# Performance work log

Hardware: AMD Instinct MI355X
Metric: run time of the kernel (lower is better)

Reference implementation:

```python
import jax, jax.numpy as jnp
import numpy as np

N_U, N_O = 20000, 10000      # rows in users / orders
C = 256                      # channels
TXT = 1536                   # text_embed_dim
NNUM, NCAT, NTXT = 3, 3, 1   # columns per stype (same for both tables)
NCOLS = NNUM + NCAT + NTXT   # 7 columns per table
VOCAB = 101                  # num_cats + 1
E = 10000                    # edges (orders -> users fkey)
MAXP = 16                    # max_parents


def setup_inputs() -> dict:
    key = jax.random.key(0)
    ks = jax.random.split(key, 24)
    s = 0.02
    return {
        "users_num": jax.random.normal(ks[0], (N_U, NNUM), jnp.float32),
        "users_cat": jax.random.randint(ks[1], (N_U, NCAT), 0, VOCAB),
        "users_text": jax.random.normal(ks[2], (N_U, NTXT, TXT), jnp.float32),
        "orders_num": jax.random.normal(ks[3], (N_O, NNUM), jnp.float32),
        "orders_cat": jax.random.randint(ks[4], (N_O, NCAT), 0, VOCAB),
        "orders_text": jax.random.normal(ks[5], (N_O, NTXT, TXT), jnp.float32),
        "edge_index": jax.random.randint(ks[6], (2, E), 0, N_O),
        "table_emb": jax.random.normal(ks[7], (2, C), jnp.float32) * s,
        # users params
        "u_num_w": jax.random.normal(ks[8], (NNUM, C), jnp.float32) * s,
        "u_num_b": jax.random.normal(ks[9], (NNUM, C), jnp.float32) * s,
        "u_cat_tab": jax.random.normal(ks[10], (NCAT, VOCAB, C), jnp.float32) * s,
        "u_txt_w": jax.random.normal(ks[11], (NTXT, C, TXT), jnp.float32) * s,
        "u_txt_b": jax.random.normal(ks[12], (NTXT, C), jnp.float32) * s,
        "u_col": jax.random.normal(ks[13], (NCOLS, C), jnp.float32) * s,
        # orders params
        "o_num_w": jax.random.normal(ks[14], (NNUM, C), jnp.float32) * s,
        "o_num_b": jax.random.normal(ks[15], (NNUM, C), jnp.float32) * s,
        "o_cat_tab": jax.random.normal(ks[16], (NCAT, VOCAB, C), jnp.float32) * s,
        "o_txt_w": jax.random.normal(ks[17], (NTXT, C, TXT), jnp.float32) * s,
        "o_txt_b": jax.random.normal(ks[18], (NTXT, C), jnp.float32) * s,
        "o_col": jax.random.normal(ks[19], (NCOLS, C), jnp.float32) * s,
    }


def _table_tokens(num, cat, txt, nw, nb, ctab, tw, tb, col, temb):
    # num: [N, NNUM]; nw/nb: [NNUM, C] -> per-col Linear(1, C) + SiLU
    tn = jax.nn.silu(num[:, :, None] * nw[None] + nb[None])        # [N, NNUM, C]
    # per-col Embedding lookup: ctab [NCAT, V, C], cat [N, NCAT]
    tc = ctab[jnp.arange(ctab.shape[0])[None, :], cat]             # [N, NCAT, C]
    # per-col Linear(TXT, C): tw [NTXT, C, TXT]
    tt = jnp.einsum('nkt,kct->nkc', txt, tw) + tb[None]            # [N, NTXT, C]
    tok = jnp.concatenate([tn, tc, tt], axis=1) + col[None] + temb  # [N, NCOLS, C]
    # original concatenates per-column blocks of N rows each -> (cols, N, C) flatten
    return tok.transpose(1, 0, 2).reshape(-1, tok.shape[-1])


def reference(users_num, users_cat, users_text, orders_num, orders_cat, orders_text,
              edge_index, table_emb,
              u_num_w, u_num_b, u_cat_tab, u_txt_w, u_txt_b, u_col,
              o_num_w, o_num_b, o_cat_tab, o_txt_w, o_txt_b, o_col):
    xu = _table_tokens(users_num, users_cat, users_text,
                       u_num_w, u_num_b, u_cat_tab, u_txt_w, u_txt_b, u_col, table_emb[0])
    xo = _table_tokens(orders_num, orders_cat, orders_text,
                       o_num_w, o_num_b, o_cat_tab, o_txt_w, o_txt_b, o_col, table_emb[1])
    x = jnp.concatenate([xu, xo], axis=0)                           # [S, C]

    node_idxs = jnp.concatenate([jnp.tile(jnp.arange(N_U), NCOLS),
                                 jnp.tile(jnp.arange(N_U, N_U + N_O), NCOLS)])
    col_idxs = jnp.concatenate([jnp.repeat(jnp.arange(NCOLS), N_U),
                                jnp.repeat(jnp.arange(NCOLS, 2 * NCOLS), N_O)])
    table_idxs = jnp.concatenate([jnp.zeros(NCOLS * N_U, jnp.int32),
                                  jnp.ones(NCOLS * N_O, jnp.int32)])

    # f2p neighbor build: first MAXP parents per child node, in edge order
    num_nodes = N_U + N_O
    child = edge_index[0] + N_U    # orders offset = N_U
    parent = edge_index[1]         # users offset = 0
    order = jnp.argsort(child, stable=True)
    cs, ps = child[order], parent[order]
    seg_start = jnp.searchsorted(cs, cs, side='left')
    rank = jnp.arange(E) - seg_start                                # position within child's group
    valid = rank < MAXP
    tbl = jnp.full((num_nodes + 1, MAXP), -1, dtype=ps.dtype)
    tbl = tbl.at[jnp.where(valid, cs, num_nodes), jnp.minimum(rank, MAXP - 1)].set(
        jnp.where(valid, ps, -1))
    f2p_nbr_idxs = tbl[:num_nodes][node_idxs]                       # [S, MAXP]

    return (x, node_idxs, col_idxs, table_idxs, f2p_nbr_idxs, num_nodes)
```

## Files before the change

kernel.cpp:

```cpp
#include <hip/hip_runtime.h>
#include <hip/hip_bf16.h>

typedef __bf16 bf16;
typedef __bf16 bf16x8 __attribute__((ext_vector_type(8)));
typedef float f32x4 __attribute__((ext_vector_type(4)));

#define NU 20000
#define NO 10000
#define CDIM 256
#define TDIM 1536
#define EN 10000
#define VOCAB 101
#define MAXP 16
#define CAP 32

#define NODE_OFF 53760000LL
#define COL_OFF  53970000LL
#define TAB_OFF  54180000LL
#define F2P_OFF  54390000LL
#define NN_OFF   57750000LL

#define GEMM_U_BLKS 314
#define GEMM_O_BLKS 158
#define MISC_BLKS   22500
#define IDX_BLKS    840
#define MISC_OFF    (GEMM_U_BLKS + GEMM_O_BLKS)
#define IDX_OFF     (MISC_OFF + MISC_BLKS)
#define TOTAL_BLKS  (IDX_OFF + IDX_BLKS)

__global__ void edges_fill(const int* __restrict__ edge, int* __restrict__ counts,
                           unsigned long long* __restrict__ pairs)
{
    int e = blockIdx.x * 256 + threadIdx.x;
    if (e >= EN) return;
    int child = edge[e];
    unsigned parent = (unsigned)edge[EN + e];
    int slot = atomicAdd(&counts[child], 1);
    if (slot < CAP)
        pairs[child * CAP + slot] = ((unsigned long long)(unsigned)e << 32) | parent;
}

__global__ void build_tbl(const int* __restrict__ counts,
                          const unsigned long long* __restrict__ pairs,
                          int* __restrict__ tbl)
{
    int mm = blockIdx.x * 256 + threadIdx.x;
    if (mm >= NO) return;
    int cnt = counts[mm];
    if (cnt > CAP) cnt = CAP;
    unsigned long long v[CAP];
    for (int i = 0; i < cnt; i++) v[i] = pairs[mm * CAP + i];
    for (int i = 1; i < cnt; i++) {
        unsigned long long key = v[i];
        int j = i - 1;
        while (j >= 0 && v[j] > key) { v[j + 1] = v[j]; j--; }
        v[j + 1] = key;
    }
#pragma unroll
    for (int j = 0; j < MAXP; j++)
        tbl[mm * MAXP + j] = (j < cnt) ? (int)(v[j] & 0xffffffffULL) : -1;
}

__device__ __forceinline__ void idx_body(int iblk, const int* __restrict__ tbl,
                                         float* __restrict__ out)
{
    int i = iblk * 256 + threadIdx.x;
    if (i >= 210000) return;
    float nodev, colvf, tabv;
    int m = -1;
    if (i < 140000) {
        int n = i % 20000;
        nodev = (float)n; colvf = (float)(i / 20000); tabv = 0.f;
    } else {
        int i2 = i - 140000;
        m = i2 % 10000;
        nodev = (float)(20000 + m); colvf = (float)(7 + i2 / 10000); tabv = 1.f;
    }
    out[NODE_OFF + i] = nodev;
    out[COL_OFF + i]  = colvf;
    out[TAB_OFF + i]  = tabv;

    float h[16];
    if (m < 0) {
#pragma unroll
        for (int j = 0; j < 16; j++) h[j] = -1.f;
    } else {
#pragma unroll
        for (int j = 0; j < 16; j++) h[j] = (float)tbl[m * MAXP + j];
    }
    float4* dst = (float4*)&out[F2P_OFF + (long long)i * 16];
#pragma unroll
    for (int j = 0; j < 4; j++)
        dst[j] = *(const float4*)&h[j * 4];
    if (i == 0) out[NN_OFF] = 30000.f;
}

__device__ __forceinline__ void misc_body(int mb,
    const float* __restrict__ unum, const int* __restrict__ ucat,
    const float* __restrict__ onum, const int* __restrict__ ocat,
    const float* __restrict__ temb,
    const float* __restrict__ unw, const float* __restrict__ unb,
    const float* __restrict__ uctab, const float* __restrict__ ucol,
    const float* __restrict__ onw, const float* __restrict__ onb,
    const float* __restrict__ octab, const float* __restrict__ ocol,
    float* __restrict__ out)
{
    int t = threadIdx.x;
    int ridx = mb * 8 + (t >> 5);
    int c0 = (t & 31) * 8;
    bool isU = ridx < 120000;
    int k, n; long long orow;
    const float *num, *nw, *nb, *ctab, *colw, *te;
    const int* cat;
    if (isU) {
        k = ridx / 20000; n = ridx - k * 20000; orow = ridx;
        num = unum; cat = ucat; nw = unw; nb = unb; ctab = uctab; colw = ucol; te = temb;
    } else {
        int i2 = ridx - 120000;
        k = i2 / 10000; n = i2 - k * 10000; orow = (long long)ridx + 20000;
        num = onum; cat = ocat; nw = onw; nb = onb; ctab = octab; colw = ocol; te = temb + CDIM;
    }
    float colv[8], tev[8];
    *(float4*)&colv[0] = *(const float4*)&colw[k * CDIM + c0];
    *(float4*)&colv[4] = *(const float4*)&colw[k * CDIM + c0 + 4];
    *(float4*)&tev[0]  = *(const float4*)&te[c0];
    *(float4*)&tev[4]  = *(const float4*)&te[c0 + 4];
    float res[8];
    if (k < 3) {
        float v = num[n * 3 + k];
        float wv[8], bv[8];
        *(float4*)&wv[0] = *(const float4*)&nw[k * CDIM + c0];
        *(float4*)&wv[4] = *(const float4*)&nw[k * CDIM + c0 + 4];
        *(float4*)&bv[0] = *(const float4*)&nb[k * CDIM + c0];
        *(float4*)&bv[4] = *(const float4*)&nb[k * CDIM + c0 + 4];
#pragma unroll
        for (int j = 0; j < 8; j++) {
            float x = v * wv[j] + bv[j];
            float s = x / (1.f + __expf(-x));
            res[j] = s + colv[j] + tev[j];
        }
    } else {
        int cv = cat[n * 3 + (k - 3)];
        float tcv[8];
        *(float4*)&tcv[0] = *(const float4*)&ctab[((k - 3) * VOCAB + cv) * CDIM + c0];
        *(float4*)&tcv[4] = *(const float4*)&ctab[((k - 3) * VOCAB + cv) * CDIM + c0 + 4];
#pragma unroll
        for (int j = 0; j < 8; j++)
            res[j] = tcv[j] + colv[j] + tev[j];
    }
    *(float4*)&out[orow * CDIM + c0]     = *(const float4*)&res[0];
    *(float4*)&out[orow * CDIM + c0 + 4] = *(const float4*)&res[4];
}

__device__ __forceinline__ void gemm_body(
    const float* __restrict__ A, const float* __restrict__ W,
    const float* __restrict__ tbias, const float* __restrict__ colw,
    const float* __restrict__ temb, float* __restrict__ out,
    int M, long long out_row_base, int mblk, int nblk,
    bf16* As, bf16* Bs)
{
    constexpr int BK = 64, LDA = 72;
    const int tid = threadIdx.x;
    const int m0 = mblk * 128;
    const int n0 = nblk * 128;
    const int w = tid >> 6, lane = tid & 63;
    const int wm = (w & 1) * 64, wn = (w >> 1) * 64;
    const int lrow = lane & 15, lquad = lane >> 4;

    f32x4 acc[4][4];
#pragma unroll
    for (int a = 0; a < 4; a++)
#pragma unroll
        for (int b = 0; b < 4; b++) acc[a][b] = (f32x4){0.f, 0.f, 0.f, 0.f};

    for (int k0 = 0; k0 < TDIM; k0 += BK) {
        __syncthreads();
#pragma unroll
        for (int i = 0; i < 8; i++) {
            int c = tid + i * 256;
            int row = c >> 4;
            int col4 = (c & 15) << 2;
            int ga = m0 + row; if (ga >= M) ga = M - 1;
            float4 av = *(const float4*)&A[(size_t)ga * TDIM + k0 + col4];
            __attribute__((aligned(8))) bf16 ha[4] =
                {(bf16)av.x, (bf16)av.y, (bf16)av.z, (bf16)av.w};
            *(unsigned long long*)&As[row * LDA + col4] = *(const unsigned long long*)ha;
            float4 bv = *(const float4*)&W[(size_t)(n0 + row) * TDIM + k0 + col4];
            __attribute__((aligned(8))) bf16 hb[4] =
                {(bf16)bv.x, (bf16)bv.y, (bf16)bv.z, (bf16)bv.w};
            *(unsigned long long*)&Bs[row * LDA + col4] = *(const unsigned long long*)hb;
        }
        __syncthreads();
#pragma unroll
        for (int ks = 0; ks < 2; ks++) {
            bf16x8 afr[4], bfr[4];
#pragma unroll
            for (int mi = 0; mi < 4; mi++)
                afr[mi] = *(const bf16x8*)&As[(wm + mi * 16 + lrow) * LDA + ks * 32 + lquad * 8];
#pragma unroll
            for (int ni = 0; ni < 4; ni++)
                bfr[ni] = *(const bf16x8*)&Bs[(wn + ni * 16 + lrow) * LDA + ks * 32 + lquad * 8];
#pragma unroll
            for (int mi = 0; mi < 4; mi++)
#pragma unroll
                for (int ni = 0; ni < 4; ni++)
                    acc[mi][ni] = __builtin_amdgcn_mfma_f32_16x16x32_bf16(
                        afr[mi], bfr[ni], acc[mi][ni], 0, 0, 0);
        }
    }

#pragma unroll
    for (int ni = 0; ni < 4; ni++) {
        int c = n0 + wn + ni * 16 + lrow;
        float bias = tbias[c] + colw[6 * CDIM + c] + temb[c];
#pragma unroll
        for (int mi = 0; mi < 4; mi++) {
            int mbase = m0 + wm + mi * 16 + lquad * 4;
#pragma unroll
            for (int r = 0; r < 4; r++) {
                int m = mbase + r;
                if (m < M)
                    out[(out_row_base + m) * CDIM + c] = acc[mi][ni][r] + bias;
            }
        }
    }
}

__global__ __launch_bounds__(256) void mega(
    const float* __restrict__ users_num, const int* __restrict__ users_cat,
    const float* __restrict__ users_text,
    const float* __restrict__ orders_num, const int* __restrict__ orders_cat,
    const float* __restrict__ orders_text,
    const float* __restrict__ temb,
    const float* __restrict__ unw, const float* __restrict__ unb,
    const float* __restrict__ uctab, const float* __restrict__ utw,
    const float* __restrict__ utb, const float* __restrict__ ucol,
    const float* __restrict__ onw, const float* __restrict__ onb,
    const float* __restrict__ octab, const float* __restrict__ otw,
    const float* __restrict__ otb, const float* __restrict__ ocol,
    const int* __restrict__ tbl, float* __restrict__ out)
{
    __shared__ bf16 As[128 * 72];
    __shared__ bf16 Bs[128 * 72];
    int b = blockIdx.x;
    if (b < GEMM_U_BLKS) {
        gemm_body(users_text, utw, utb, ucol, temb, out,
                  NU, 120000LL, b >> 1, b & 1, As, Bs);
    } else if (b < MISC_OFF) {
        int bb = b - GEMM_U_BLKS;
        gemm_body(orders_text, otw, otb, ocol, temb + CDIM, out,
                  NO, 200000LL, bb >> 1, bb & 1, As, Bs);
    } else if (b < IDX_OFF) {
        misc_body(b - MISC_OFF, users_num, users_cat, orders_num, orders_cat,
                  temb, unw, unb, uctab, ucol, onw, onb, octab, ocol, out);
    } else {
        idx_body(b - IDX_OFF, tbl, out);
    }
}

extern "C" void kernel_launch(void* const* d_in, const int* in_sizes, int n_in,
                              void* d_out, int out_size, void* d_ws, size_t ws_size,
                              hipStream_t stream)
{
    const float* users_num   = (const float*)d_in[0];
    const int*   users_cat   = (const int*)d_in[1];
    const float* users_text  = (const float*)d_in[2];
    const float* orders_num  = (const float*)d_in[3];
    const int*   orders_cat  = (const int*)d_in[4];
    const float* orders_text = (const float*)d_in[5];
    const int*   edge_index  = (const int*)d_in[6];
    const float* table_emb   = (const float*)d_in[7];
    const float* u_num_w   = (const float*)d_in[8];
    const float* u_num_b   = (const float*)d_in[9];
    const float* u_cat_tab = (const float*)d_in[10];
    const float* u_txt_w   = (const float*)d_in[11];
    const float* u_txt_b   = (const float*)d_in[12];
    const float* u_col     = (const float*)d_in[13];
    const float* o_num_w   = (const float*)d_in[14];
    const float* o_num_b   = (const float*)d_in[15];
    const float* o_cat_tab = (const float*)d_in[16];
    const float* o_txt_w   = (const float*)d_in[17];
    const float* o_txt_b   = (const float*)d_in[18];
    const float* o_col     = (const float*)d_in[19];
    float* out = (float*)d_out;

    int* counts = (int*)d_ws;
    unsigned long long* pairs = (unsigned long long*)((char*)d_ws + 65536);
    int* tbl = (int*)((char*)d_ws + 65536 + (size_t)NO * CAP * 8);

    hipMemsetAsync(counts, 0, NO * sizeof(int), stream);
    edges_fill<<<(EN + 255) / 256, 256, 0, stream>>>(edge_index, counts, pairs);
    build_tbl<<<(NO + 255) / 256, 256, 0, stream>>>(counts, pairs, tbl);
    mega<<<TOTAL_BLKS, 256, 0, stream>>>(
        users_num, users_cat, users_text, orders_num, orders_cat, orders_text,
        table_emb, u_num_w, u_num_b, u_cat_tab, u_txt_w, u_txt_b, u_col,
        o_num_w, o_num_b, o_cat_tab, o_txt_w, o_txt_b, o_col, tbl, out);
}
```

Before: 479.6 us.

## Pre-convert text and weights to bf16 and stream GEMM tiles via direct LDS loads

A new prep kernel converts the user and order text activations and the text weights from fp32 to bf16 in workspace, fused with the edge-fill step. The GEMM then loads bf16 tiles straight into LDS with global_load_lds, so it no longer converts in registers during the main loop and reads half the bytes. The cost is an extra pass that reads the full fp32 text once and writes a bf16 copy of roughly 90 MB. The old fp32 path is kept as a fallback for when the workspace is too small.

```diff
diff --git a/kernel.cpp b/kernel.cpp
--- a/kernel.cpp
+++ b/kernel.cpp
@@ -28,10 +28,26 @@
 #define IDX_OFF     (MISC_OFF + MISC_BLKS)
 #define TOTAL_BLKS  (IDX_OFF + IDX_BLKS)
 
-__global__ void edges_fill(const int* __restrict__ edge, int* __restrict__ counts,
-                           unsigned long long* __restrict__ pairs)
-{
-    int e = blockIdx.x * 256 + threadIdx.x;
+#define P_EDGE  40
+#define P_CVU   (P_EDGE + 7500)
+#define P_CVO   (P_CVU + 3750)
+#define P_CVWU  (P_CVO + 96)
+#define P_CVWO  (P_CVWU + 96)
+#define PREP_BLKS P_CVWO
+
+#define WS_PAIRS_OFF 65536ULL
+#define WS_TBL_OFF   (WS_PAIRS_OFF + (unsigned long long)NO * CAP * 8)
+#define WS_AB_U_OFF  (WS_TBL_OFF + (unsigned long long)NO * MAXP * 4)
+#define WS_AB_O_OFF  (WS_AB_U_OFF + (unsigned long long)NU * TDIM * 2)
+#define WS_WB_U_OFF  (WS_AB_O_OFF + (unsigned long long)NO * TDIM * 2)
+#define WS_WB_O_OFF  (WS_WB_U_OFF + (unsigned long long)CDIM * TDIM * 2)
+#define WS_NEED      (WS_WB_O_OFF + (unsigned long long)CDIM * TDIM * 2)
+
+__device__ __forceinline__ void edges_body(int eblk, const int* __restrict__ edge,
+                                           int* __restrict__ counts,
+                                           unsigned long long* __restrict__ pairs)
+{
+    int e = eblk * 256 + threadIdx.x;
     if (e >= EN) return;
     int child = edge[e];
     unsigned parent = (unsigned)edge[EN + e];
@@ -59,6 +75,38 @@
 #pragma unroll
     for (int j = 0; j < MAXP; j++)
         tbl[mm * MAXP + j] = (j < cnt) ? (int)(v[j] & 0xffffffffULL) : -1;
+}
+
+__device__ __forceinline__ void conv_body(const float* __restrict__ src,
+                                          bf16* __restrict__ dst, int relblk)
+{
+    long long e = (long long)relblk * 4096 + (long long)threadIdx.x * 16;
+    float4 f0 = *(const float4*)&src[e];
+    float4 f1 = *(const float4*)&src[e + 4];
+    float4 f2 = *(const float4*)&src[e + 8];
+    float4 f3 = *(const float4*)&src[e + 12];
+    bf16x8 h0 = {(bf16)f0.x, (bf16)f0.y, (bf16)f0.z, (bf16)f0.w,
+                 (bf16)f1.x, (bf16)f1.y, (bf16)f1.z, (bf16)f1.w};
+    bf16x8 h1 = {(bf16)f2.x, (bf16)f2.y, (bf16)f2.z, (bf16)f2.w,
+                 (bf16)f3.x, (bf16)f3.y, (bf16)f3.z, (bf16)f3.w};
+    *(bf16x8*)&dst[e]     = h0;
+    *(bf16x8*)&dst[e + 8] = h1;
+}
+
+__global__ __launch_bounds__(256) void prep(
+    const int* __restrict__ edge, int* __restrict__ counts,
+    unsigned long long* __restrict__ pairs,
+    const float* __restrict__ users_text, const float* __restrict__ orders_text,
+    const float* __restrict__ utw, const float* __restrict__ otw,
+    bf16* __restrict__ AbU, bf16* __restrict__ AbO,
+    bf16* __restrict__ WbU, bf16* __restrict__ WbO)
+{
+    int b = blockIdx.x;
+    if (b < P_EDGE)       edges_body(b, edge, counts, pairs);
+    else if (b < P_CVU)   conv_body(users_text,  AbU, b - P_EDGE);
+    else if (b < P_CVO)   conv_body(orders_text, AbO, b - P_CVU);
+    else if (b < P_CVWU)  conv_body(utw, WbU, b - P_CVO);
+    else                  conv_body(otw, WbO, b - P_CVWU);
 }
 
 __device__ __forceinline__ void idx_body(int iblk, const int* __restrict__ tbl,
@@ -152,14 +200,20 @@
     *(float4*)&out[orow * CDIM + c0 + 4] = *(const float4*)&res[4];
 }
 
-__device__ __forceinline__ void gemm_body(
-    const float* __restrict__ A, const float* __restrict__ W,
+__device__ __forceinline__ void gload16(const void* g, void* l)
+{
+    __builtin_amdgcn_global_load_lds(
+        (const __attribute__((address_space(1))) void*)g,
+        (__attribute__((address_space(3))) void*)l, 16, 0, 0);
+}
+
+__device__ __forceinline__ void gemm_bf16_body(
+    const bf16* __restrict__ A, const bf16* __restrict__ W,
     const float* __restrict__ tbias, const float* __restrict__ colw,
     const float* __restrict__ temb, float* __restrict__ out,
     int M, long long out_row_base, int mblk, int nblk,
     bf16* As, bf16* Bs)
 {
-    constexpr int BK = 64, LDA = 72;
     const int tid = threadIdx.x;
     const int m0 = mblk * 128;
     const int n0 = nblk * 128;
@@ -173,7 +227,74 @@
 #pragma unroll
         for (int b = 0; b < 4; b++) acc[a][b] = (f32x4){0.f, 0.f, 0.f, 0.f};
 
-    for (int k0 = 0; k0 < TDIM; k0 += BK) {
+    for (int k0 = 0; k0 < TDIM; k0 += 64) {
+        __syncthreads();
+#pragma unroll
+        for (int i = 0; i < 4; i++) {
+            int ch = i * 256 + w * 64 + lane;
+            int row = ch >> 3, col8 = (ch & 7) * 8;
+            int ga = m0 + row; if (ga >= M) ga = M - 1;
+            gload16(&A[(size_t)ga * TDIM + k0 + col8], &As[(size_t)(i * 256 + w * 64) * 8]);
+            gload16(&W[(size_t)(n0 + row) * TDIM + k0 + col8], &Bs[(size_t)(i * 256 + w * 64) * 8]);
+        }
+        __syncthreads();
+#pragma unroll
+        for (int ks = 0; ks < 2; ks++) {
+            bf16x8 afr[4], bfr[4];
+#pragma unroll
+            for (int mi = 0; mi < 4; mi++)
+                afr[mi] = *(const bf16x8*)&As[(wm + mi * 16 + lrow) * 64 + ks * 32 + lquad * 8];
+#pragma unroll
+            for (int ni = 0; ni < 4; ni++)
+                bfr[ni] = *(const bf16x8*)&Bs[(wn + ni * 16 + lrow) * 64 + ks * 32 + lquad * 8];
+#pragma unroll
+            for (int mi = 0; mi < 4; mi++)
+#pragma unroll
+                for (int ni = 0; ni < 4; ni++)
+                    acc[mi][ni] = __builtin_amdgcn_mfma_f32_16x16x32_bf16(
+                        afr[mi], bfr[ni], acc[mi][ni], 0, 0, 0);
+        }
+    }
+
+#pragma unroll
+    for (int ni = 0; ni < 4; ni++) {
+        int c = n0 + wn + ni * 16 + lrow;
+        float bias = tbias[c] + colw[6 * CDIM + c] + temb[c];
+#pragma unroll
+        for (int mi = 0; mi < 4; mi++) {
+            int mbase = m0 + wm + mi * 16 + lquad * 4;
+#pragma unroll
+            for (int r = 0; r < 4; r++) {
+                int m = mbase + r;
+                if (m < M)
+                    out[(out_row_base + m) * CDIM + c] = acc[mi][ni][r] + bias;
+            }
+        }
+    }
+}
+
+__device__ __forceinline__ void gemm_f32_body(
+    const float* __restrict__ A, const float* __restrict__ W,
+    const float* __restrict__ tbias, const float* __restrict__ colw,
+    const float* __restrict__ temb, float* __restrict__ out,
+    int M, long long out_row_base, int mblk, int nblk,
+    bf16* As, bf16* Bs)
+{
+    constexpr int LDA = 72;
+    const int tid = threadIdx.x;
+    const int m0 = mblk * 128;
+    const int n0 = nblk * 128;
+    const int w = tid >> 6, lane = tid & 63;
+    const int wm = (w & 1) * 64, wn = (w >> 1) * 64;
+    const int lrow = lane & 15, lquad = lane >> 4;
+
+    f32x4 acc[4][4];
+#pragma unroll
+    for (int a = 0; a < 4; a++)
+#pragma unroll
+        for (int b = 0; b < 4; b++) acc[a][b] = (f32x4){0.f, 0.f, 0.f, 0.f};
+
+    for (int k0 = 0; k0 < TDIM; k0 += 64) {
         __syncthreads();
 #pragma unroll
         for (int i = 0; i < 8; i++) {
@@ -228,6 +349,38 @@
 
 __global__ __launch_bounds__(256) void mega(
     const float* __restrict__ users_num, const int* __restrict__ users_cat,
+    const float* __restrict__ orders_num, const int* __restrict__ orders_cat,
+    const float* __restrict__ temb,
+    const float* __restrict__ unw, const float* __restrict__ unb,
+    const float* __restrict__ uctab,
+    const float* __restrict__ utb, const float* __restrict__ ucol,
+    const float* __restrict__ onw, const float* __restrict__ onb,
+    const float* __restrict__ octab,
+    const float* __restrict__ otb, const float* __restrict__ ocol,
+    const bf16* __restrict__ AbU, const bf16* __restrict__ AbO,
+    const bf16* __restrict__ WbU, const bf16* __restrict__ WbO,
+    const int* __restrict__ tbl, float* __restrict__ out)
+{
+    __shared__ bf16 As[128 * 64];
+    __shared__ bf16 Bs[128 * 64];
+    int b = blockIdx.x;
+    if (b < GEMM_U_BLKS) {
+        gemm_bf16_body(AbU, WbU, utb, ucol, temb, out,
+                       NU, 120000LL, b >> 1, b & 1, As, Bs);
+    } else if (b < MISC_OFF) {
+        int bb = b - GEMM_U_BLKS;
+        gemm_bf16_body(AbO, WbO, otb, ocol, temb + CDIM, out,
+                       NO, 200000LL, bb >> 1, bb & 1, As, Bs);
+    } else if (b < IDX_OFF) {
+        misc_body(b - MISC_OFF, users_num, users_cat, orders_num, orders_cat,
+                  temb, unw, unb, uctab, ucol, onw, onb, octab, ocol, out);
+    } else {
+        idx_body(b - IDX_OFF, tbl, out);
+    }
+}
+
+__global__ __launch_bounds__(256) void mega_fb(
+    const float* __restrict__ users_num, const int* __restrict__ users_cat,
     const float* __restrict__ users_text,
     const float* __restrict__ orders_num, const int* __restrict__ orders_cat,
     const float* __restrict__ orders_text,
@@ -244,18 +397,24 @@
     __shared__ bf16 Bs[128 * 72];
     int b = blockIdx.x;
     if (b < GEMM_U_BLKS) {
-        gemm_body(users_text, utw, utb, ucol, temb, out,
-                  NU, 120000LL, b >> 1, b & 1, As, Bs);
+        gemm_f32_body(users_text, utw, utb, ucol, temb, out,
+                      NU, 120000LL, b >> 1, b & 1, As, Bs);
     } else if (b < MISC_OFF) {
         int bb = b - GEMM_U_BLKS;
-        gemm_body(orders_text, otw, otb, ocol, temb + CDIM, out,
-                  NO, 200000LL, bb >> 1, bb & 1, As, Bs);
+        gemm_f32_body(orders_text, otw, otb, ocol, temb + CDIM, out,
+                      NO, 200000LL, bb >> 1, bb & 1, As, Bs);
     } else if (b < IDX_OFF) {
         misc_body(b - MISC_OFF, users_num, users_cat, orders_num, orders_cat,
                   temb, unw, unb, uctab, ucol, onw, onb, octab, ocol, out);
     } else {
         idx_body(b - IDX_OFF, tbl, out);
     }
+}
+
+__global__ void edges_fill(const int* __restrict__ edge, int* __restrict__ counts,
+                           unsigned long long* __restrict__ pairs)
+{
+    edges_body(blockIdx.x, edge, counts, pairs);
 }
 
 extern "C" void kernel_launch(void* const* d_in, const int* in_sizes, int n_in,
@@ -285,14 +444,30 @@
     float* out = (float*)d_out;
 
     int* counts = (int*)d_ws;
-    unsigned long long* pairs = (unsigned long long*)((char*)d_ws + 65536);
-    int* tbl = (int*)((char*)d_ws + 65536 + (size_t)NO * CAP * 8);
+    unsigned long long* pairs = (unsigned long long*)((char*)d_ws + WS_PAIRS_OFF);
+    int* tbl = (int*)((char*)d_ws + WS_TBL_OFF);
 
     hipMemsetAsync(counts, 0, NO * sizeof(int), stream);
-    edges_fill<<<(EN + 255) / 256, 256, 0, stream>>>(edge_index, counts, pairs);
-    build_tbl<<<(NO + 255) / 256, 256, 0, stream>>>(counts, pairs, tbl);
-    mega<<<TOTAL_BLKS, 256, 0, stream>>>(
-        users_num, users_cat, users_text, orders_num, orders_cat, orders_text,
-        table_emb, u_num_w, u_num_b, u_cat_tab, u_txt_w, u_txt_b, u_col,
-        o_num_w, o_num_b, o_cat_tab, o_txt_w, o_txt_b, o_col, tbl, out);
-}
+
+    if (ws_size >= WS_NEED) {
+        bf16* AbU = (bf16*)((char*)d_ws + WS_AB_U_OFF);
+        bf16* AbO = (bf16*)((char*)d_ws + WS_AB_O_OFF);
+        bf16* WbU = (bf16*)((char*)d_ws + WS_WB_U_OFF);
+        bf16* WbO = (bf16*)((char*)d_ws + WS_WB_O_OFF);
+        prep<<<PREP_BLKS, 256, 0, stream>>>(edge_index, counts, pairs,
+            users_text, orders_text, u_txt_w, o_txt_w, AbU, AbO, WbU, WbO);
+        build_tbl<<<(NO + 255) / 256, 256, 0, stream>>>(counts, pairs, tbl);
+        mega<<<TOTAL_BLKS, 256, 0, stream>>>(
+            users_num, users_cat, orders_num, orders_cat,
+            table_emb, u_num_w, u_num_b, u_cat_tab, u_txt_b, u_col,
+            o_num_w, o_num_b, o_cat_tab, o_txt_b, o_col,
+            AbU, AbO, WbU, WbO, tbl, out);
+    } else {
+        edges_fill<<<P_EDGE, 256, 0, stream>>>(edge_index, counts, pairs);
+        build_tbl<<<(NO + 255) / 256, 256, 0, stream>>>(counts, pairs, tbl);
+        mega_fb<<<TOTAL_BLKS, 256, 0, stream>>>(
+            users_num, users_cat, users_text, orders_num, orders_cat, orders_text,
+            table_emb, u_num_w, u_num_b, u_cat_tab, u_txt_w, u_txt_b, u_col,
+            o_num_w, o_num_b, o_cat_tab, o_txt_w, o_txt_b, o_col, tbl, out);
+    }
+}
```

Measured after the change: 493.2 us. +2.8%, slower.
